# Kernel tuning notes

Hardware: AMD Instinct MI355X
Metric: run time of the kernel (lower is better)

The kernel has to match this reference:

```python
import jax, jax.numpy as jnp
import numpy as np
from jax import lax


def setup_inputs() -> dict:
    key = jax.random.key(0)
    x = jax.random.normal(key, (4, 8192, 3), dtype=jnp.float32)
    return {"x": x, "k": 16}


def reference(x, k):
    p = x[..., :3]                                  # (B, N, 3)
    # Brute-force KNN: squared euclidean distances (B, N, N)
    sq = jnp.sum(p * p, axis=-1)                    # (B, N)
    d2 = sq[:, :, None] + sq[:, None, :] - 2.0 * jnp.einsum('bnd,bmd->bnm', p, p)
    _, idx = lax.top_k(-d2, k)                      # (B, N, k), nearest (incl. self)
    # Gather neighbors per batch
    neighbors = jax.vmap(lambda pts, ids: pts[ids])(p, idx)   # (B, N, k, 3)
    mean = jnp.mean(neighbors, axis=2, keepdims=True)          # (B, N, 1, 3)
    diff = neighbors - mean                                    # (B, N, k, 3)
    # cov = mean_k (diff diff^T) over neighbors -> (B, N, 3, 3)
    cov = jnp.einsum('bnki,bnkj->bnij', diff, diff) / k
    ev = jnp.linalg.eigvalsh(cov)                  # ascending: (B, N, 3)
    lambda0 = ev[..., 2]
    lambda1 = ev[..., 1]
    return lambda0 / lambda1
```

## Files before the change

### kernel.cpp

```cpp
#include <hip/hip_runtime.h>
#include <math.h>

#define NB 4
#define NP 8192
#define KK 16
#define QPB 64
#define NPTS (NB * NP)

#define TSAMP 2048
#define TCH 256
#define NTS 8
#define BCH 1024
#define NBCH 8
#define CAP 30
#define SROW 34
#define SCH (64 * SROW + 2)
#define PADKEY 0xFFFFFFFFFFFFFFFFull

#define CSWAP_DESC(a, b) { float _lo = fminf(a, b); float _hi = fmaxf(a, b); a = _hi; b = _lo; }
#define CSWAP_ASC(a, b)  { float _lo = fminf(a, b); float _hi = fmaxf(a, b); a = _lo; b = _hi; }

__device__ __forceinline__ float ref_sq(float x, float y, float z) {
  return __fadd_rn(__fadd_rn(__fmul_rn(x, x), __fmul_rn(y, y)), __fmul_rn(z, z));
}

__device__ __forceinline__ float ref_d2q(float qx, float qy, float qz, float sqq,
                                         float4 c) {
  float dot = __fadd_rn(__fadd_rn(__fmul_rn(qx, c.x), __fmul_rn(qy, c.y)),
                        __fmul_rn(qz, c.z));
  float s = __fadd_rn(sqq, c.w);
  return __fmaf_rn(-2.0f, dot, s);
}

__device__ __forceinline__ unsigned int ord_f32(float d) {
  unsigned int b = __float_as_uint(d);
  return b ^ ((b >> 31) ? 0xFFFFFFFFu : 0x80000000u);
}

__device__ __forceinline__ double eigen_ratio_tail(
    float cxx, float cyy, float czz, float cxy, float cxz, float cyz,
    float k1) {
  double a   = (double)__fmul_rn(cxx, k1), b = (double)__fmul_rn(cyy, k1);
  double c2  = (double)__fmul_rn(czz, k1);
  double dxy = (double)__fmul_rn(cxy, k1), exz = (double)__fmul_rn(cxz, k1);
  double fyz = (double)__fmul_rn(cyz, k1);
  double qm = (a + b + c2) / 3.0;
  double p1 = dxy * dxy + exz * exz + fyz * fyz;
  double aa = a - qm, bb = b - qm, cc = c2 - qm;
  double p2 = aa * aa + bb * bb + cc * cc + 2.0 * p1;
  if (p2 <= 0.0) return 1.0;
  double p  = sqrt(p2 / 6.0);
  double ip = 1.0 / p;
  double b00 = aa * ip, b11 = bb * ip, b22 = cc * ip;
  double b01 = dxy * ip, b02 = exz * ip, b12 = fyz * ip;
  double detB = b00 * (b11 * b22 - b12 * b12)
              - b01 * (b01 * b22 - b12 * b02)
              + b02 * (b01 * b12 - b11 * b02);
  double r = 0.5 * detB;
  r = fmin(1.0, fmax(-1.0, r));
  const double dcl = 2.0 * r;
  float phif = acosf((float)r) * (1.0f / 3.0f);
  double y0 = 2.0 * (double)cosf(phif);
  double y2 = 2.0 * (double)cosf(phif + 2.0943951f);
#pragma unroll
  for (int it = 0; it < 3; ++it) {
    double g0 = 3.0 * (y0 * y0 - 1.0);
    if (fabs(g0) > 1e-4) y0 -= (y0 * y0 * y0 - 3.0 * y0 - dcl) / g0;
    double g2 = 3.0 * (y2 * y2 - 1.0);
    if (fabs(g2) > 1e-4) y2 -= (y2 * y2 * y2 - 3.0 * y2 - dcl) / g2;
  }
  double e0 = qm + p * y0;
  double e2v = qm + p * y2;
  double e1 = 3.0 * qm - e0 - e2v;
  return e0 / e1;
}

__device__ __forceinline__ void topk_update(float bd[KK], float d[8]) {
  CSWAP_DESC(d[0], d[1]) CSWAP_DESC(d[2], d[3]) CSWAP_DESC(d[4], d[5]) CSWAP_DESC(d[6], d[7])
  CSWAP_DESC(d[0], d[2]) CSWAP_DESC(d[1], d[3]) CSWAP_DESC(d[4], d[6]) CSWAP_DESC(d[5], d[7])
  CSWAP_DESC(d[1], d[2]) CSWAP_DESC(d[5], d[6])
  CSWAP_DESC(d[0], d[4]) CSWAP_DESC(d[1], d[5]) CSWAP_DESC(d[2], d[6]) CSWAP_DESC(d[3], d[7])
  CSWAP_DESC(d[2], d[4]) CSWAP_DESC(d[3], d[5])
  CSWAP_DESC(d[1], d[2]) CSWAP_DESC(d[3], d[4]) CSWAP_DESC(d[5], d[6])
#pragma unroll
  for (int i = 0; i < 8; ++i) bd[8 + i] = fminf(bd[8 + i], d[i]);
#pragma unroll
  for (int i = 0; i < 8; ++i)  CSWAP_ASC(bd[i], bd[i + 8])
#pragma unroll
  for (int i = 0; i < 4; ++i)  CSWAP_ASC(bd[i], bd[i + 4])
#pragma unroll
  for (int i = 8; i < 12; ++i) CSWAP_ASC(bd[i], bd[i + 4])
#pragma unroll
  for (int g = 0; g < 4; ++g) {
    CSWAP_ASC(bd[4 * g + 0], bd[4 * g + 2]) CSWAP_ASC(bd[4 * g + 1], bd[4 * g + 3])
    CSWAP_ASC(bd[4 * g + 0], bd[4 * g + 1]) CSWAP_ASC(bd[4 * g + 2], bd[4 * g + 3])
  }
}

__global__ void prep_kernel(const float* __restrict__ x,
                            float4* __restrict__ cand) {
  int i = blockIdx.x * 256 + threadIdx.x;
  if (i < NPTS) {
    float px = x[3 * i + 0], py = x[3 * i + 1], pz = x[3 * i + 2];
    cand[i] = make_float4(px, py, pz, ref_sq(px, py, pz));
  }
}

__global__ __launch_bounds__(512) void tau_stage_kernel(
    const float4* __restrict__ cand, float* __restrict__ tauArr) {
  __shared__ __align__(16) char smem[NTS * 64 * 17 * 4];
  float4* samp = (float4*)smem;
  float (*s_t)[64][17] = (float (*)[64][17])smem;
  const int tid   = threadIdx.x;
  const int lane  = tid & 63;
  const int w     = __builtin_amdgcn_readfirstlane(tid >> 6);
  const int group = blockIdx.x;
  const int batch = group >> 7;
  const int qbase = (group & 127) * QPB;
  const float4* __restrict__ Cb = cand + (size_t)batch * NP;

  const float4 q = Cb[qbase + lane];
  const float qx = q.x, qy = q.y, qz = q.z, sqq = q.w;

#pragma unroll
  for (int r = 0; r < TSAMP / 512; ++r)
    samp[r * 512 + tid] = Cb[r * 512 + tid];
  __syncthreads();

  float bd[KK];
#pragma unroll
  for (int t = 0; t < KK; ++t) bd[t] = 3.4e38f;

  const int j0 = w * TCH;
  for (int jj = 0; jj < TCH; jj += 8) {
    const float4* xp = samp + (j0 + jj);
    float4 c[8];
#pragma unroll
    for (int u = 0; u < 8; ++u) c[u] = xp[u];
    float d[8];
#pragma unroll
    for (int u = 0; u < 8; ++u) d[u] = ref_d2q(qx, qy, qz, sqq, c[u]);
    topk_update(bd, d);
  }
  __syncthreads();

#pragma unroll
  for (int t = 0; t < KK; ++t) s_t[w][lane][t] = bd[t];
  __syncthreads();

  if (w == 0) {
    float md[KK];
#pragma unroll
    for (int t = 0; t < KK; ++t) md[t] = s_t[0][lane][t];
#pragma unroll
    for (int s2 = 1; s2 < NTS; ++s2) {
      float d[KK];
#pragma unroll
      for (int t = 0; t < KK; ++t) d[t] = s_t[s2][lane][t];
      topk_update(md, &d[0]);
      topk_update(md, &d[8]);
    }
    tauArr[batch * NP + qbase + lane] = md[KK - 1];
  }
}

__global__ __launch_bounds__(512) void filter_select_kernel(
    const float4* __restrict__ cand, const float* __restrict__ tauArr,
    float* __restrict__ out) {
  extern __shared__ __align__(16) char smem[];
  unsigned short* s_idx = (unsigned short*)smem;
  unsigned long long* keys = (unsigned long long*)smem;
  unsigned short* s_cnt = (unsigned short*)(smem + 65536);

  const int tid   = threadIdx.x;
  const int lane  = tid & 63;
  const int w     = __builtin_amdgcn_readfirstlane(tid >> 6);
  const int group = blockIdx.x;
  const int batch = group >> 7;
  const int qbase = (group & 127) * QPB;
  const float4* __restrict__ Cb = cand + (size_t)batch * NP;

  {
    const int j0 = w * BCH;
    const float tau = tauArr[batch * NP + qbase + lane];
    const float4 q = Cb[qbase + lane];
    const float qx = q.x, qy = q.y, qz = q.z, sqq = q.w;

    unsigned short* Srow = &s_idx[w * SCH + lane * SROW];
    int cnt = 0;
    for (int jj = 0; jj < BCH; jj += 16) {
      const float4* xp = Cb + (j0 + jj);
      float4 c[16];
#pragma unroll
      for (int u = 0; u < 16; ++u) c[u] = xp[u];
#pragma unroll
      for (int u = 0; u < 16; ++u) {
        float d = ref_d2q(qx, qy, qz, sqq, c[u]);
        if (d <= tau) {
          if (cnt < CAP) Srow[1 + cnt] = (unsigned short)(j0 + jj + u);
          ++cnt;
        }
      }
    }
    s_cnt[w * 64 + lane] = (unsigned short)cnt;
  }
  __syncthreads();

  const int qlq = tid >> 3;
  const int pch = tid & 7;
  unsigned long long slots[KK];
#pragma unroll
  for (int t = 0; t < KK; ++t) slots[t] = PADKEY;
  {
    const float4 qq = Cb[qbase + qlq];
    const float q2x = qq.x, q2y = qq.y, q2z = qq.z, sq2 = qq.w;
    const unsigned short* row = &s_idx[pch * SCH + qlq * SROW + 1];
    int cnl = (int)s_cnt[pch * 64 + qlq];
    if (cnl > CAP) cnl = CAP;
    for (int e = 0; e < cnl; e += 8) {
      unsigned long long kv[8];
#pragma unroll
      for (int u = 0; u < 8; ++u) {
        const bool ok = (e + u) < cnl;
        const int j = ok ? (int)row[e + u] : 0;
        const float dd = ref_d2q(q2x, q2y, q2z, sq2, Cb[j]);
        kv[u] = ok ? ((((unsigned long long)ord_f32(dd)) << 32) |
                      (unsigned int)j)
                   : PADKEY;
      }
#pragma unroll
      for (int u = 0; u < 8; ++u) {
        const unsigned long long k = kv[u];
        if (k < slots[KK - 1]) {
#pragma unroll
          for (int t = KK - 1; t >= 1; --t) {
            unsigned long long lo =
                (slots[t] < k) ? slots[t] : k;
            slots[t] = (slots[t - 1] > lo) ? slots[t - 1] : lo;
          }
          slots[0] = (slots[0] < k) ? slots[0] : k;
        }
      }
    }
  }
  __syncthreads();

#pragma unroll
  for (int t = 0; t < KK; ++t)
    keys[((qlq << 3) + pch) * KK + t] = slots[t];
  __syncthreads();

  if (tid < QPB) {
    const int ql = tid;
    const int qg = batch * NP + qbase + ql;
    const float4 qq = Cb[qbase + ql];
    const float q2x = qq.x, q2y = qq.y, q2z = qq.z, sq2 = qq.w;

    int total = 0;
    bool fs = false;
#pragma unroll
    for (int p = 0; p < NBCH; ++p) {
      const int c = (int)s_cnt[p * 64 + ql];
      if (c > CAP) fs = true;
      total += c;
    }
    if (total < KK) fs = true;

    int mjr[KK];
    if (!fs) {
      const unsigned long long* kq = keys + (ql << 3) * KK;
      int head[NBCH];
#pragma unroll
      for (int p = 0; p < NBCH; ++p) head[p] = 0;
#pragma unroll
      for (int t = 0; t < KK; ++t) {
        unsigned long long best = PADKEY;
        int bp = 0;
#pragma unroll
        for (int p = 0; p < NBCH; ++p) {
          const unsigned long long k =
              (head[p] < KK) ? kq[p * KK + head[p]] : PADKEY;
          if (k < best) { best = k; bp = p; }
        }
        head[bp]++;
        mjr[t] = (int)(best & 0xFFFFull);
      }
    } else {
      float md[KK];
#pragma unroll
      for (int t = 0; t < KK; ++t) { md[t] = 3.4e38f; mjr[t] = 0; }
      for (int j = 0; j < NP; ++j) {
        float d = ref_d2q(q2x, q2y, q2z, sq2, Cb[j]);
        if (d < md[KK - 1]) {
          bool c0 = d < md[0];
#pragma unroll
          for (int t = KK - 1; t >= 1; --t) {
            bool cl = d < md[t];
            bool cp = d < md[t - 1];
            float nv = fmaxf(md[t - 1], fminf(md[t], d));
            mjr[t] = cl ? (cp ? mjr[t - 1] : j) : mjr[t];
            md[t] = nv;
          }
          mjr[0] = c0 ? j : mjr[0];
          md[0] = fminf(md[0], d);
        }
      }
    }

    float4 pts[KK];
#pragma unroll
    for (int s = 0; s < KK; ++s) pts[s] = Cb[mjr[s]];

    float sx = 0.f, sy = 0.f, sz = 0.f;
#pragma unroll
    for (int s = 0; s < KK; ++s) {
      sx = __fadd_rn(sx, pts[s].x);
      sy = __fadd_rn(sy, pts[s].y);
      sz = __fadd_rn(sz, pts[s].z);
    }
    const float k1 = 1.0f / KK;
    const float mx = sx * k1, my = sy * k1, mz = sz * k1;

    float cxx = 0.f, cxy = 0.f, cxz = 0.f, cyy = 0.f, cyz = 0.f, czz = 0.f;
#pragma unroll
    for (int s = 0; s < KK; ++s) {
      float dx = __fsub_rn(pts[s].x, mx);
      float dy = __fsub_rn(pts[s].y, my);
      float dz = __fsub_rn(pts[s].z, mz);
      cxx = __fadd_rn(cxx, __fmul_rn(dx, dx));
      cxy = __fadd_rn(cxy, __fmul_rn(dx, dy));
      cxz = __fadd_rn(cxz, __fmul_rn(dx, dz));
      cyy = __fadd_rn(cyy, __fmul_rn(dy, dy));
      cyz = __fadd_rn(cyz, __fmul_rn(dy, dz));
      czz = __fadd_rn(czz, __fmul_rn(dz, dz));
    }

    out[qg] = (float)eigen_ratio_tail(cxx, cyy, czz, cxy, cxz, cyz, k1);
  }
}

__global__ __launch_bounds__(512, 4) void knn_eigen_fallback(
    const float4* __restrict__ cand, float* __restrict__ out) {
  __shared__ unsigned short s_j[8][QPB][18];

  const int tid   = threadIdx.x;
  const int lane  = tid & 63;
  const int w     = __builtin_amdgcn_readfirstlane(tid >> 6);
  const int batch = blockIdx.x >> 7;
  const int qbase = (blockIdx.x & 127) * QPB;
  const int FCH   = NP / 8;

  const float4* __restrict__ Cb = cand + (size_t)batch * NP;

  const float4 q = Cb[qbase + lane];
  const float qx = q.x, qy = q.y, qz = q.z, sqq = q.w;

  float bd[KK];
#pragma unroll
  for (int t = 0; t < KK; ++t) bd[t] = 3.4e38f;

  const int j0 = w * FCH;
  for (int jj = 0; jj < FCH; jj += 8) {
    const float4* xp = Cb + (j0 + jj);
    float4 c[8];
#pragma unroll
    for (int u = 0; u < 8; ++u) c[u] = xp[u];
    float d[8];
#pragma unroll
    for (int u = 0; u < 8; ++u) d[u] = ref_d2q(qx, qy, qz, sqq, c[u]);
    topk_update(bd, d);
  }

  const float T = bd[KK - 1];
  int cnt = 0;
  for (int jj = 0; jj < FCH; jj += 8) {
    const float4* xp = Cb + (j0 + jj);
    float4 c[8];
#pragma unroll
    for (int u = 0; u < 8; ++u) c[u] = xp[u];
#pragma unroll
    for (int u = 0; u < 8; ++u) {
      float d = ref_d2q(qx, qy, qz, sqq, c[u]);
      if (d <= T && cnt < KK) {
        s_j[w][lane][cnt] = (unsigned short)(j0 + jj + u);
        cnt++;
      }
    }
  }
  __syncthreads();

  if (tid < QPB) {
    const float4 qq = Cb[qbase + tid];
    const float q2x = qq.x, q2y = qq.y, q2z = qq.z, sq2 = qq.w;
    float md[KK]; int mj[KK];
#pragma unroll
    for (int t = 0; t < KK; ++t) { md[t] = 3.4e38f; mj[t] = 0; }
    for (int cch = 0; cch < 8; ++cch) {
      const unsigned int* rowp = (const unsigned int*)&s_j[cch][tid][0];
#pragma unroll
      for (int sp = 0; sp < KK / 2; ++sp) {
        unsigned int pk = rowp[sp];
#pragma unroll
        for (int half = 0; half < 2; ++half) {
          int j = (half == 0) ? (int)(pk & 0xFFFFu) : (int)(pk >> 16);
          float d = ref_d2q(q2x, q2y, q2z, sq2, Cb[j]);
          if (d < md[KK - 1]) {
            bool c0 = d < md[0];
#pragma unroll
            for (int t = KK - 1; t >= 1; --t) {
              bool cl = d < md[t];
              bool cp = d < md[t - 1];
              float nv = fmaxf(md[t - 1], fminf(md[t], d));
              mj[t] = cl ? (cp ? mj[t - 1] : j) : mj[t];
              md[t] = nv;
            }
            mj[0] = c0 ? j : mj[0];
            md[0] = fminf(md[0], d);
          }
        }
      }
    }
    float sx = 0.f, sy = 0.f, sz = 0.f;
#pragma unroll
    for (int s = 0; s < KK; ++s) {
      float4 pp = Cb[mj[s]];
      sx = __fadd_rn(sx, pp.x);
      sy = __fadd_rn(sy, pp.y);
      sz = __fadd_rn(sz, pp.z);
    }
    const float k1 = 1.0f / KK;
    const float mx = sx * k1, my = sy * k1, mz = sz * k1;
    float cxx = 0.f, cxy = 0.f, cxz = 0.f, cyy = 0.f, cyz = 0.f, czz = 0.f;
#pragma unroll
    for (int s = 0; s < KK; ++s) {
      float4 pp = Cb[mj[s]];
      float dx = __fsub_rn(pp.x, mx);
      float dy = __fsub_rn(pp.y, my);
      float dz = __fsub_rn(pp.z, mz);
      cxx = __fadd_rn(cxx, __fmul_rn(dx, dx));
      cxy = __fadd_rn(cxy, __fmul_rn(dx, dy));
      cxz = __fadd_rn(cxz, __fmul_rn(dx, dz));
      cyy = __fadd_rn(cyy, __fmul_rn(dy, dy));
      cyz = __fadd_rn(cyz, __fmul_rn(dy, dz));
      czz = __fadd_rn(czz, __fmul_rn(dz, dz));
    }
    out[(size_t)batch * NP + qbase + tid] =
        (float)eigen_ratio_tail(cxx, cyy, czz, cxy, cxz, cyz, k1);
  }
}

extern "C" void kernel_launch(void* const* d_in, const int* in_sizes, int n_in,
                              void* d_out, int out_size, void* d_ws, size_t ws_size,
                              hipStream_t stream) {
  const float* x = (const float*)d_in[0];
  float* out = (float*)d_out;
  float4* cand = (float4*)d_ws;
  float* tauArr = (float*)((char*)d_ws + (size_t)NPTS * sizeof(float4));
  const size_t need = (size_t)NPTS * sizeof(float4) +
                      (size_t)NPTS * sizeof(float);

  prep_kernel<<<dim3(NPTS / 256), dim3(256), 0, stream>>>(x, cand);
  if (ws_size >= need) {
    tau_stage_kernel<<<dim3(512), dim3(512), 0, stream>>>(cand, tauArr);
    const size_t fs_lds = 65536 + 1024;
    filter_select_kernel<<<dim3(512), dim3(512), fs_lds, stream>>>(
        cand, tauArr, out);
  } else {
    knn_eigen_fallback<<<dim3(NPTS / QPB), dim3(512), 0, stream>>>(cand, out);
  }
}
```

Measured before the change: 200.7 us.

## Use FMA distances with tau margin, dual top-k chains, and padded key layout

The tau stage now splits candidate scanning into two independent top-k chains that are merged at the end, which should raise instruction-level parallelism. Distance computation in the tau and filter passes uses fused multiply-adds, and a small margin is added to tau so that rounding differences cannot drop true neighbours. The shared key buffer gets padded strides (17 per chunk plus one per query) to cut LDS bank conflicts during the merge. The cost is higher LDS use, which may lower occupancy, and the margin may let slightly more candidates through the filter.

```diff
diff --git a/kernel.cpp b/kernel.cpp
--- a/kernel.cpp
+++ b/kernel.cpp
@@ -15,7 +15,10 @@
 #define CAP 30
 #define SROW 34
 #define SCH (64 * SROW + 2)
+#define KCH 17
+#define KQS (NBCH * KCH + 1)
 #define PADKEY 0xFFFFFFFFFFFFFFFFull
+#define TAU_MARGIN 2.5e-4f
 
 #define CSWAP_DESC(a, b) { float _lo = fminf(a, b); float _hi = fmaxf(a, b); a = _hi; b = _lo; }
 #define CSWAP_ASC(a, b)  { float _lo = fminf(a, b); float _hi = fmaxf(a, b); a = _lo; b = _hi; }
@@ -28,6 +31,13 @@
                                          float4 c) {
   float dot = __fadd_rn(__fadd_rn(__fmul_rn(qx, c.x), __fmul_rn(qy, c.y)),
                         __fmul_rn(qz, c.z));
+  float s = __fadd_rn(sqq, c.w);
+  return __fmaf_rn(-2.0f, dot, s);
+}
+
+__device__ __forceinline__ float fast_d2(float qx, float qy, float qz, float sqq,
+                                         float4 c) {
+  float dot = __fmaf_rn(qz, c.z, __fmaf_rn(qy, c.y, __fmul_rn(qx, c.x)));
   float s = __fadd_rn(sqq, c.w);
   return __fmaf_rn(-2.0f, dot, s);
 }
@@ -127,25 +137,30 @@
     samp[r * 512 + tid] = Cb[r * 512 + tid];
   __syncthreads();
 
-  float bd[KK];
-#pragma unroll
-  for (int t = 0; t < KK; ++t) bd[t] = 3.4e38f;
+  float bdA[KK], bdB[KK];
+#pragma unroll
+  for (int t = 0; t < KK; ++t) { bdA[t] = 3.4e38f; bdB[t] = 3.4e38f; }
 
   const int j0 = w * TCH;
-  for (int jj = 0; jj < TCH; jj += 8) {
+  for (int jj = 0; jj < TCH; jj += 16) {
     const float4* xp = samp + (j0 + jj);
-    float4 c[8];
-#pragma unroll
-    for (int u = 0; u < 8; ++u) c[u] = xp[u];
-    float d[8];
-#pragma unroll
-    for (int u = 0; u < 8; ++u) d[u] = ref_d2q(qx, qy, qz, sqq, c[u]);
-    topk_update(bd, d);
-  }
-  __syncthreads();
-
-#pragma unroll
-  for (int t = 0; t < KK; ++t) s_t[w][lane][t] = bd[t];
+    float4 c[16];
+#pragma unroll
+    for (int u = 0; u < 16; ++u) c[u] = xp[u];
+    float dA[8], dB[8];
+#pragma unroll
+    for (int u = 0; u < 8; ++u) dA[u] = fast_d2(qx, qy, qz, sqq, c[u]);
+#pragma unroll
+    for (int u = 0; u < 8; ++u) dB[u] = fast_d2(qx, qy, qz, sqq, c[8 + u]);
+    topk_update(bdA, dA);
+    topk_update(bdB, dB);
+  }
+  topk_update(bdA, &bdB[0]);
+  topk_update(bdA, &bdB[8]);
+  __syncthreads();
+
+#pragma unroll
+  for (int t = 0; t < KK; ++t) s_t[w][lane][t] = bdA[t];
   __syncthreads();
 
   if (w == 0) {
@@ -170,7 +185,7 @@
   extern __shared__ __align__(16) char smem[];
   unsigned short* s_idx = (unsigned short*)smem;
   unsigned long long* keys = (unsigned long long*)smem;
-  unsigned short* s_cnt = (unsigned short*)(smem + 65536);
+  unsigned short* s_cnt = (unsigned short*)(smem + 70144);
 
   const int tid   = threadIdx.x;
   const int lane  = tid & 63;
@@ -182,7 +197,7 @@
 
   {
     const int j0 = w * BCH;
-    const float tau = tauArr[batch * NP + qbase + lane];
+    const float tau = tauArr[batch * NP + qbase + lane] + TAU_MARGIN;
     const float4 q = Cb[qbase + lane];
     const float qx = q.x, qy = q.y, qz = q.z, sqq = q.w;
 
@@ -195,7 +210,7 @@
       for (int u = 0; u < 16; ++u) c[u] = xp[u];
 #pragma unroll
       for (int u = 0; u < 16; ++u) {
-        float d = ref_d2q(qx, qy, qz, sqq, c[u]);
+        float d = fast_d2(qx, qy, qz, sqq, c[u]);
         if (d <= tau) {
           if (cnt < CAP) Srow[1 + cnt] = (unsigned short)(j0 + jj + u);
           ++cnt;
@@ -247,7 +262,7 @@
 
 #pragma unroll
   for (int t = 0; t < KK; ++t)
-    keys[((qlq << 3) + pch) * KK + t] = slots[t];
+    keys[qlq * KQS + pch * KCH + t] = slots[t];
   __syncthreads();
 
   if (tid < QPB) {
@@ -268,7 +283,7 @@
 
     int mjr[KK];
     if (!fs) {
-      const unsigned long long* kq = keys + (ql << 3) * KK;
+      const unsigned long long* kq = keys + ql * KQS;
       int head[NBCH];
 #pragma unroll
       for (int p = 0; p < NBCH; ++p) head[p] = 0;
@@ -279,7 +294,7 @@
 #pragma unroll
         for (int p = 0; p < NBCH; ++p) {
           const unsigned long long k =
-              (head[p] < KK) ? kq[p * KK + head[p]] : PADKEY;
+              (head[p] < KK) ? kq[p * KCH + head[p]] : PADKEY;
           if (k < best) { best = k; bp = p; }
         }
         head[bp]++;
@@ -462,7 +477,7 @@
   prep_kernel<<<dim3(NPTS / 256), dim3(256), 0, stream>>>(x, cand);
   if (ws_size >= need) {
     tau_stage_kernel<<<dim3(512), dim3(512), 0, stream>>>(cand, tauArr);
-    const size_t fs_lds = 65536 + 1024;
+    const size_t fs_lds = 70144 + 1024;
     filter_select_kernel<<<dim3(512), dim3(512), fs_lds, stream>>>(
         cand, tauArr, out);
   } else {
```

Result: faster. 187.6 us (-6.5%).
